# Performance work log

Hardware: AMD Instinct MI355X
Metric: run time of the kernel (lower is better)

The kernel has to match this reference:

```python
import jax, jax.numpy as jnp
import numpy as np

B, S, D, H = 2, 2048, 1024, 16
HD = D // H  # 64


def setup_inputs() -> dict:
    key = jax.random.key(0)
    ks = jax.random.split(key, 10)
    sc = 1.0 / np.sqrt(D)
    return {
        "decoder_hs": jax.random.normal(ks[0], (B, S, D), jnp.float32),
        "encoder_hs": jax.random.normal(ks[1], (B, S, D), jnp.float32),
        "Wq": jax.random.normal(ks[2], (D, D), jnp.float32) * sc,
        "bq": jax.random.normal(ks[3], (D,), jnp.float32) * 0.02,
        "Wk": jax.random.normal(ks[4], (D, D), jnp.float32) * sc,
        "bk": jax.random.normal(ks[5], (D,), jnp.float32) * 0.02,
        "Wv": jax.random.normal(ks[6], (D, D), jnp.float32) * sc,
        "bv": jax.random.normal(ks[7], (D,), jnp.float32) * 0.02,
        "Wp": jax.random.normal(ks[8], (D, D), jnp.float32) * sc,
        "bp": jax.random.normal(ks[9], (D,), jnp.float32) * 0.02,
    }


def reference(decoder_hs, encoder_hs, Wq, bq, Wk, bk, Wv, bv, Wp, bp):
    b, s, d = decoder_hs.shape
    # torch nn.Linear: y = x @ W.T + b, W is [out, in]
    q = decoder_hs @ Wq.T + bq
    k = encoder_hs @ Wk.T + bk
    v = encoder_hs @ Wv.T + bv
    # head split: [b, s, d] -> [b, h, s, hd]
    q = q.reshape(b, s, H, HD).transpose(0, 2, 1, 3)
    k = k.reshape(b, s, H, HD).transpose(0, 2, 1, 3)
    v = v.reshape(b, s, H, HD).transpose(0, 2, 1, 3)
    scale = 1.0 / np.sqrt(HD).astype(np.float32)
    att = jnp.einsum('bhqd,bhkd->bhqk', q, k) * scale
    att = jax.nn.softmax(att, axis=-1)
    y = jnp.einsum('bhqk,bhkd->bhqd', att, v)
    y = y.transpose(0, 2, 1, 3).reshape(b, s, d)
    return y @ Wp.T + bp
```

## Files before the change

kernel.cpp:

```cpp
#include <hip/hip_runtime.h>
#include <hip/hip_bf16.h>
#include <cstdint>
#include <cstddef>

#define BB 2
#define SS 2048
#define DD 1024
#define HH 16
#define HD 64

typedef __attribute__((ext_vector_type(8))) short bf16x8;
typedef __attribute__((ext_vector_type(4))) short bf16x4;
typedef __attribute__((ext_vector_type(4))) float f32x4;

#define MFMA16(va, vb, c) __builtin_amdgcn_mfma_f32_16x16x16bf16_1k(va, vb, c, 0, 0, 0)

#define GLL(g, l) __builtin_amdgcn_global_load_lds( \
    (const __attribute__((address_space(1))) void*)(g), \
    (__attribute__((address_space(3))) void*)(l), 16, 0, 0)

__device__ __forceinline__ short f2bf_fast(float f) {
    uint32_t u = __float_as_uint(f);
    u += 0x7FFF + ((u >> 16) & 1);
    return (short)(u >> 16);
}
__device__ __forceinline__ uint32_t pack_bf2(float a, float b) {
    uint32_t ua = __float_as_uint(a), ub = __float_as_uint(b);
    ua += 0x7FFF + ((ua >> 16) & 1);
    ub += 0x7FFF + ((ub >> 16) & 1);
    return (ua >> 16) | (ub & 0xFFFF0000u);
}
__device__ __forceinline__ bf16x8 cvt8(const float* __restrict__ p) {
    float4 a = *(const float4*)p;
    float4 b = *(const float4*)(p + 4);
    union { uint32_t d[4]; bf16x8 v; } r;
    r.d[0] = pack_bf2(a.x, a.y);
    r.d[1] = pack_bf2(a.z, a.w);
    r.d[2] = pack_bf2(b.x, b.y);
    r.d[3] = pack_bf2(b.z, b.w);
    return r.v;
}

__global__ __launch_bounds__(256) void cvt6_kernel(
    const float* __restrict__ s0, const float* __restrict__ s1,
    const float* __restrict__ s2, const float* __restrict__ s3,
    const float* __restrict__ s4, const float* __restrict__ s5,
    short* __restrict__ d0, short* __restrict__ d1, short* __restrict__ d2,
    short* __restrict__ d3, short* __restrict__ d4, short* __restrict__ d5)
{
    const int z = blockIdx.z;
    const float* s = (z == 0) ? s0 : (z == 1) ? s1 : (z == 2) ? s2
                   : (z == 3) ? s3 : (z == 4) ? s4 : s5;
    short* d = (z == 0) ? d0 : (z == 1) ? d1 : (z == 2) ? d2
             : (z == 3) ? d3 : (z == 4) ? d4 : d5;
    const int n8 = (z < 2) ? (BB * SS * DD / 8) : (DD * DD / 8);
    const int id = blockIdx.x * 256 + threadIdx.x;
    if (id >= n8) return;
    bf16x8 r = cvt8(s + (size_t)id * 8);
    *(uint4*)(d + (size_t)id * 8) = *(uint4*)&r;
}

template<int BF>
__global__ __launch_bounds__(256, 3) void qkv_gemm_kernel(
    const void* __restrict__ dec, const void* __restrict__ enc,
    const void* __restrict__ Wq, const void* __restrict__ Wk,
    const void* __restrict__ Wv,
    const float* __restrict__ bq, const float* __restrict__ bk,
    const float* __restrict__ bv,
    short* __restrict__ Qo, short* __restrict__ Ko, short* __restrict__ Vo)
{
    __shared__ short As[128 * 32];
    __shared__ short Bs[128 * 32];

    const int z = blockIdx.z;
    const void* Xv = (z == 0) ? dec : enc;
    const void* Wp_ = (z == 0) ? Wq : (z == 1) ? Wk : Wv;
    const float* bias = (z == 0) ? bq : (z == 1) ? bk : bv;
    short* Yo = (z == 0) ? Qo : (z == 1) ? Ko : Vo;

    const int t = threadIdx.x;
    const int lane = t & 63, wv = t >> 6;
    const int lr = lane & 15, quad = lane >> 4;
    const int wm = wv >> 1, wn = wv & 1;
    const int m0 = blockIdx.y * 128;
    const int n0 = blockIdx.x * 128;
    const int K = DD;

    f32x4 acc[4][4];
    #pragma unroll
    for (int i = 0; i < 4; i++)
        #pragma unroll
        for (int j = 0; j < 4; j++) acc[i][j] = (f32x4){0.f, 0.f, 0.f, 0.f};

    for (int kb = 0; kb < K; kb += 32) {
        __syncthreads();
        if (BF) {
            const short* Xb = (const short*)Xv;
            const short* Wb = (const short*)Wp_;
            #pragma unroll
            for (int c = 0; c < 2; c++) {
                int r0 = wv * 32 + c * 16;
                int r = r0 + (lane >> 2), ch = (lane & 3) * 8;
                GLL(Xb + (size_t)(m0 + r) * K + kb + ch, &As[r0 * 32]);
                GLL(Wb + (size_t)(n0 + r) * K + kb + ch, &Bs[r0 * 32]);
            }
        } else {
            const float* Xf = (const float*)Xv;
            const float* Wf = (const float*)Wp_;
            #pragma unroll
            for (int c = 0; c < 2; c++) {
                int id = t + c * 256;
                int r = id >> 2, c8 = (id & 3) * 8;
                *(bf16x8*)&As[r * 32 + c8] = cvt8(Xf + (size_t)(m0 + r) * K + kb + c8);
                *(bf16x8*)&Bs[r * 32 + c8] = cvt8(Wf + (size_t)(n0 + r) * K + kb + c8);
            }
        }
        __syncthreads();

        bf16x8 af[4], bfr[4];
        #pragma unroll
        for (int mi = 0; mi < 4; mi++)
            af[mi] = *(const bf16x8*)&As[(wm * 64 + mi * 16 + lr) * 32 + quad * 8];
        #pragma unroll
        for (int ni = 0; ni < 4; ni++)
            bfr[ni] = *(const bf16x8*)&Bs[(wn * 64 + ni * 16 + lr) * 32 + quad * 8];
        #pragma unroll
        for (int mi = 0; mi < 4; mi++)
            #pragma unroll
            for (int ni = 0; ni < 4; ni++)
                acc[mi][ni] = __builtin_amdgcn_mfma_f32_16x16x32_bf16(
                    af[mi], bfr[ni], acc[mi][ni], 0, 0, 0);
    }

    if (z < 2) {
        #pragma unroll
        for (int ni = 0; ni < 4; ni++) {
            int col = n0 + wn * 64 + ni * 16 + lr;
            int h = col >> 6, hd = col & 63;
            float bvv = bias[col];
            #pragma unroll
            for (int mi = 0; mi < 4; mi++) {
                #pragma unroll
                for (int r2 = 0; r2 < 4; r2++) {
                    int row = m0 + wm * 64 + mi * 16 + quad * 4 + r2;
                    int b = row >> 11, s = row & 2047;
                    float v = acc[mi][ni][r2] + bvv;
                    size_t off = ((size_t)(b * HH + h) * SS + s) * HD + hd;
                    Yo[off] = f2bf_fast(v);
                }
            }
        }
    } else {
        #pragma unroll
        for (int ni = 0; ni < 4; ni++) {
            int col = n0 + wn * 64 + ni * 16 + lr;
            int h = col >> 6, hd = col & 63;
            float bvv = bias[col];
            #pragma unroll
            for (int mi = 0; mi < 4; mi++) {
                int s0 = m0 + wm * 64 + mi * 16 + quad * 4;
                int b = s0 >> 11, s = s0 & 2047;
                union { uint32_t d[2]; } u;
                u.d[0] = pack_bf2(acc[mi][ni][0] + bvv, acc[mi][ni][1] + bvv);
                u.d[1] = pack_bf2(acc[mi][ni][2] + bvv, acc[mi][ni][3] + bvv);
                size_t off = ((size_t)(b * HH + h) * HD + hd) * SS + s;
                *(uint2*)(Yo + off) = *(uint2*)&u;
            }
        }
    }
}

template<int WBF>
__global__ __launch_bounds__(256, 2) void proj_gemm_kernel(
    const short* __restrict__ X,
    const void* __restrict__ W, const float* __restrict__ bias,
    float* __restrict__ Y)
{
    __shared__ short As[64 * 32];
    __shared__ short Bs[128 * 32];

    const int t = threadIdx.x;
    const int lane = t & 63, wv = t >> 6;
    const int lr = lane & 15, quad = lane >> 4;
    const int wm = wv >> 1, wn = wv & 1;
    const int m0 = blockIdx.y * 64;
    const int n0 = blockIdx.x * 128;
    const int K = DD, N = DD;

    f32x4 acc[2][4];
    #pragma unroll
    for (int i = 0; i < 2; i++)
        #pragma unroll
        for (int j = 0; j < 4; j++) acc[i][j] = (f32x4){0.f, 0.f, 0.f, 0.f};

    for (int kb = 0; kb < K; kb += 32) {
        __syncthreads();
        {
            int r0 = wv * 16;
            int r = r0 + (lane >> 2), ch = (lane & 3) * 8;
            GLL(X + (size_t)(m0 + r) * K + kb + ch, &As[r0 * 32]);
        }
        if (WBF) {
            const short* Wb = (const short*)W;
            #pragma unroll
            for (int c = 0; c < 2; c++) {
                int r0 = wv * 32 + c * 16;
                int r = r0 + (lane >> 2), ch = (lane & 3) * 8;
                GLL(Wb + (size_t)(n0 + r) * K + kb + ch, &Bs[r0 * 32]);
            }
        } else {
            const float* Wf = (const float*)W;
            #pragma unroll
            for (int c = 0; c < 2; c++) {
                int id = t + c * 256;
                int r = id >> 2, c8 = (id & 3) * 8;
                *(bf16x8*)&Bs[r * 32 + c8] = cvt8(Wf + (size_t)(n0 + r) * K + kb + c8);
            }
        }
        __syncthreads();

        bf16x8 af[2], bfr[4];
        #pragma unroll
        for (int mi = 0; mi < 2; mi++)
            af[mi] = *(const bf16x8*)&As[(wm * 32 + mi * 16 + lr) * 32 + quad * 8];
        #pragma unroll
        for (int ni = 0; ni < 4; ni++)
            bfr[ni] = *(const bf16x8*)&Bs[(wn * 64 + ni * 16 + lr) * 32 + quad * 8];
        #pragma unroll
        for (int mi = 0; mi < 2; mi++)
            #pragma unroll
            for (int ni = 0; ni < 4; ni++)
                acc[mi][ni] = __builtin_amdgcn_mfma_f32_16x16x32_bf16(
                    af[mi], bfr[ni], acc[mi][ni], 0, 0, 0);
    }

    #pragma unroll
    for (int ni = 0; ni < 4; ni++) {
        int col = n0 + wn * 64 + ni * 16 + lr;
        float bvv = bias[col];
        #pragma unroll
        for (int mi = 0; mi < 2; mi++) {
            #pragma unroll
            for (int r2 = 0; r2 < 4; r2++) {
                int row = m0 + wm * 32 + mi * 16 + quad * 4 + r2;
                Y[(size_t)row * N + col] = acc[mi][ni][r2] + bvv;
            }
        }
    }
}

__global__ __launch_bounds__(256, 2) void attn_kernel(
    const short* __restrict__ Q,
    const short* __restrict__ Kgl,
    const short* __restrict__ Vt_g,
    short* __restrict__ Y)
{
    __shared__ short Ks[128][72];
    __shared__ short Vt[64][136];

    const int t = threadIdx.x;
    const int lane = t & 63, w = t >> 6;
    const int lr = lane & 15, quad = lane >> 4;

    const int qt = blockIdx.x & 15;
    const int bh = blockIdx.x >> 4;
    const int b = bh >> 4, h = bh & 15;

    const float C = 0.125f * 1.44269504088896f;

    const short* QpA = Q + ((size_t)bh * SS + qt * 128 + w * 32 + lr) * HD;
    const short* QpB = QpA + 16 * HD;
    bf16x8 qfA0 = *(const bf16x8*)(QpA + quad * 8);
    bf16x8 qfA1 = *(const bf16x8*)(QpA + 32 + quad * 8);
    bf16x8 qfB0 = *(const bf16x8*)(QpB + quad * 8);
    bf16x8 qfB1 = *(const bf16x8*)(QpB + 32 + quad * 8);

    f32x4 oA[4], oB[4];
    #pragma unroll
    for (int i = 0; i < 4; i++) {
        oA[i] = (f32x4){0.f, 0.f, 0.f, 0.f};
        oB[i] = (f32x4){0.f, 0.f, 0.f, 0.f};
    }
    float lsumA = 0.f, lsumB = 0.f;

    const uint4* Kg0 = (const uint4*)(Kgl + (size_t)bh * SS * HD);
    const short* Vg0 = Vt_g + (size_t)bh * HD * SS;

    for (int kt = 0; kt < SS / 128; kt++) {
        __syncthreads();
        const uint4* Kg = Kg0 + (size_t)kt * 128 * 8;
        #pragma unroll
        for (int c = 0; c < 4; c++) {
            int id = t + c * 256;
            int row = id >> 3, h8 = id & 7;
            *(uint4*)&Ks[row][h8 * 8] = Kg[id];
        }
        #pragma unroll
        for (int c = 0; c < 4; c++) {
            int id = t + c * 256;
            int hd = id >> 4, s16 = id & 15;
            *(uint4*)&Vt[hd][s16 * 8] =
                *(const uint4*)(Vg0 + (size_t)hd * SS + kt * 128 + s16 * 8);
        }
        __syncthreads();

        f32x4 scA[8], scB[8];
        #pragma unroll
        for (int nt = 0; nt < 8; nt++) {
            bf16x8 kf0 = *(const bf16x8*)&Ks[nt * 16 + lr][quad * 8];
            bf16x8 kf1 = *(const bf16x8*)&Ks[nt * 16 + lr][32 + quad * 8];
            scA[nt] = __builtin_amdgcn_mfma_f32_16x16x32_bf16(
                kf0, qfA0, (f32x4){0.f, 0.f, 0.f, 0.f}, 0, 0, 0);
            scA[nt] = __builtin_amdgcn_mfma_f32_16x16x32_bf16(kf1, qfA1, scA[nt], 0, 0, 0);
            scB[nt] = __builtin_amdgcn_mfma_f32_16x16x32_bf16(
                kf0, qfB0, (f32x4){0.f, 0.f, 0.f, 0.f}, 0, 0, 0);
            scB[nt] = __builtin_amdgcn_mfma_f32_16x16x32_bf16(kf1, qfB1, scB[nt], 0, 0, 0);
        }

        bf16x4 pbA[8], pbB[8];
        #pragma unroll
        for (int nt = 0; nt < 8; nt++) {
            float a0 = __builtin_amdgcn_exp2f(scA[nt][0] * C);
            float a1 = __builtin_amdgcn_exp2f(scA[nt][1] * C);
            float a2 = __builtin_amdgcn_exp2f(scA[nt][2] * C);
            float a3 = __builtin_amdgcn_exp2f(scA[nt][3] * C);
            lsumA += (a0 + a1) + (a2 + a3);
            union { uint32_t d[2]; bf16x4 v; } ua;
            ua.d[0] = pack_bf2(a0, a1);
            ua.d[1] = pack_bf2(a2, a3);
            pbA[nt] = ua.v;
            float b0 = __builtin_amdgcn_exp2f(scB[nt][0] * C);
            float b1 = __builtin_amdgcn_exp2f(scB[nt][1] * C);
            float b2 = __builtin_amdgcn_exp2f(scB[nt][2] * C);
            float b3 = __builtin_amdgcn_exp2f(scB[nt][3] * C);
            lsumB += (b0 + b1) + (b2 + b3);
            union { uint32_t d[2]; bf16x4 v; } ub;
            ub.d[0] = pack_bf2(b0, b1);
            ub.d[1] = pack_bf2(b2, b3);
            pbB[nt] = ub.v;
        }

        #pragma unroll
        for (int dt = 0; dt < 4; dt++) {
            #pragma unroll
            for (int nt = 0; nt < 8; nt++) {
                bf16x4 va = *(const bf16x4*)&Vt[dt * 16 + lr][nt * 16 + quad * 4];
                oA[dt] = MFMA16(va, pbA[nt], oA[dt]);
                oB[dt] = MFMA16(va, pbB[nt], oB[dt]);
            }
        }
    }

    lsumA += __shfl_xor(lsumA, 16, 64);
    lsumA += __shfl_xor(lsumA, 32, 64);
    lsumB += __shfl_xor(lsumB, 16, 64);
    lsumB += __shfl_xor(lsumB, 32, 64);
    float invA = 1.0f / lsumA, invB = 1.0f / lsumB;

    const int srowA = qt * 128 + w * 32 + lr;
    short* YpA = Y + ((size_t)b * SS + srowA) * DD + h * 64 + quad * 4;
    short* YpB = YpA + 16 * DD;
    #pragma unroll
    for (int dt = 0; dt < 4; dt++) {
        union { uint32_t d[2]; } ua;
        ua.d[0] = pack_bf2(oA[dt][0] * invA, oA[dt][1] * invA);
        ua.d[1] = pack_bf2(oA[dt][2] * invA, oA[dt][3] * invA);
        *(uint2*)(YpA + dt * 16) = *(uint2*)&ua;
        union { uint32_t d[2]; } ub;
        ub.d[0] = pack_bf2(oB[dt][0] * invB, oB[dt][1] * invB);
        ub.d[1] = pack_bf2(oB[dt][2] * invB, oB[dt][3] * invB);
        *(uint2*)(YpB + dt * 16) = *(uint2*)&ub;
    }
}

extern "C" void kernel_launch(void* const* d_in, const int* in_sizes, int n_in,
                              void* d_out, int out_size, void* d_ws, size_t ws_size,
                              hipStream_t stream) {
    const float* dec = (const float*)d_in[0];
    const float* enc = (const float*)d_in[1];
    const float* Wq  = (const float*)d_in[2];
    const float* bq  = (const float*)d_in[3];
    const float* Wk  = (const float*)d_in[4];
    const float* bk  = (const float*)d_in[5];
    const float* Wv  = (const float*)d_in[6];
    const float* bv  = (const float*)d_in[7];
    const float* Wp  = (const float*)d_in[8];
    const float* bp  = (const float*)d_in[9];

    const size_t per = (size_t)BB * HH * SS * HD;
    const size_t wsz = (size_t)DD * DD;
    short* ws = (short*)d_ws;
    short* Qb  = ws;
    short* Kb  = ws + per;
    short* Vtb = ws + 2 * per;
    short* Yb  = ws + 3 * per;

    dim3 qkv_grid(DD / 128, (BB * SS) / 128, 3);
    dim3 proj_grid(DD / 128, (BB * SS) / 64);
    const int attn_blocks = BB * HH * (SS / 128);

    const size_t need = (6 * per + 4 * wsz) * sizeof(short);
    if (ws_size >= need) {
        short* decb = ws + 4 * per;
        short* encb = ws + 5 * per;
        short* Wqb  = ws + 6 * per;
        short* Wkb  = Wqb + wsz;
        short* Wvb  = Wqb + 2 * wsz;
        short* Wpb  = Wqb + 3 * wsz;
        cvt6_kernel<<<dim3((BB * SS * DD / 8 + 255) / 256, 1, 6), 256, 0, stream>>>(
            dec, enc, Wq, Wk, Wv, Wp, decb, encb, Wqb, Wkb, Wvb, Wpb);
        qkv_gemm_kernel<1><<<qkv_grid, 256, 0, stream>>>(
            decb, encb, Wqb, Wkb, Wvb, bq, bk, bv, Qb, Kb, Vtb);
        attn_kernel<<<attn_blocks, 256, 0, stream>>>(Qb, Kb, Vtb, Yb);
        proj_gemm_kernel<1><<<proj_grid, 256, 0, stream>>>(Yb, Wpb, bp, (float*)d_out);
    } else {
        qkv_gemm_kernel<0><<<qkv_grid, 256, 0, stream>>>(
            dec, enc, Wq, Wk, Wv, bq, bk, bv, Qb, Kb, Vtb);
        attn_kernel<<<attn_blocks, 256, 0, stream>>>(Qb, Kb, Vtb, Yb);
        proj_gemm_kernel<0><<<proj_grid, 256, 0, stream>>>(Yb, Wp, bp, (float*)d_out);
    }
}
```

Measured before the change: 215.8 us.

## Double-buffer K/V tiles with async global-to-LDS loads and XOR swizzle

After: 212.3 us. About the same (-1.6%).

```diff
diff --git a/kernel.cpp b/kernel.cpp
--- a/kernel.cpp
+++ b/kernel.cpp
@@ -255,15 +255,18 @@
     const short* __restrict__ Vt_g,
     short* __restrict__ Y)
 {
-    __shared__ short Ks[128][72];
-    __shared__ short Vt[64][136];
+    __shared__ short Ks[2][128][64];
+    __shared__ short Vt[2][64][128];
 
     const int t = threadIdx.x;
     const int lane = t & 63, w = t >> 6;
     const int lr = lane & 15, quad = lane >> 4;
-
-    const int qt = blockIdx.x & 15;
-    const int bh = blockIdx.x >> 4;
+    const int e = lr & 7;
+
+    const int bid = blockIdx.x;
+    const int slot = bid >> 3;
+    const int bh = ((slot >> 4) << 3) + (bid & 7);
+    const int qt = slot & 15;
     const int b = bh >> 4, h = bh & 15;
 
     const float C = 0.125f * 1.44269504088896f;
@@ -283,32 +286,39 @@
     }
     float lsumA = 0.f, lsumB = 0.f;
 
-    const uint4* Kg0 = (const uint4*)(Kgl + (size_t)bh * SS * HD);
-    const short* Vg0 = Vt_g + (size_t)bh * HD * SS;
-
+    const short* Kb = Kgl + (size_t)bh * SS * HD;
+    const short* Vb = Vt_g + (size_t)bh * HD * SS;
+
+    auto stage = [&](int kt1, int nb) {
+        #pragma unroll
+        for (int c = 0; c < 4; c++) {
+            int r0 = w * 32 + c * 8;
+            int r  = r0 + (lane >> 3);
+            int sc = ((lane & 7) ^ (r & 7)) * 8;
+            GLL(Kb + (size_t)(kt1 * 128 + r) * 64 + sc, &Ks[nb][r0][0]);
+        }
+        #pragma unroll
+        for (int c = 0; c < 4; c++) {
+            int h0 = w * 16 + c * 4;
+            int hd = h0 + (lane >> 4);
+            int s16 = (lane & 15) ^ (hd & 7);
+            GLL(Vb + (size_t)hd * SS + kt1 * 128 + s16 * 8, &Vt[nb][h0][0]);
+        }
+    };
+
+    stage(0, 0);
+    __syncthreads();
+
+    int cur = 0;
     for (int kt = 0; kt < SS / 128; kt++) {
-        __syncthreads();
-        const uint4* Kg = Kg0 + (size_t)kt * 128 * 8;
-        #pragma unroll
-        for (int c = 0; c < 4; c++) {
-            int id = t + c * 256;
-            int row = id >> 3, h8 = id & 7;
-            *(uint4*)&Ks[row][h8 * 8] = Kg[id];
-        }
-        #pragma unroll
-        for (int c = 0; c < 4; c++) {
-            int id = t + c * 256;
-            int hd = id >> 4, s16 = id & 15;
-            *(uint4*)&Vt[hd][s16 * 8] =
-                *(const uint4*)(Vg0 + (size_t)hd * SS + kt * 128 + s16 * 8);
-        }
-        __syncthreads();
+        if (kt + 1 < SS / 128) stage(kt + 1, cur ^ 1);
 
         f32x4 scA[8], scB[8];
         #pragma unroll
         for (int nt = 0; nt < 8; nt++) {
-            bf16x8 kf0 = *(const bf16x8*)&Ks[nt * 16 + lr][quad * 8];
-            bf16x8 kf1 = *(const bf16x8*)&Ks[nt * 16 + lr][32 + quad * 8];
+            const short* krow = &Ks[cur][nt * 16 + lr][0];
+            bf16x8 kf0 = *(const bf16x8*)&krow[(quad ^ e) * 8];
+            bf16x8 kf1 = *(const bf16x8*)&krow[((quad + 4) ^ e) * 8];
             scA[nt] = __builtin_amdgcn_mfma_f32_16x16x32_bf16(
                 kf0, qfA0, (f32x4){0.f, 0.f, 0.f, 0.f}, 0, 0, 0);
             scA[nt] = __builtin_amdgcn_mfma_f32_16x16x32_bf16(kf1, qfA1, scA[nt], 0, 0, 0);
@@ -342,13 +352,18 @@
 
         #pragma unroll
         for (int dt = 0; dt < 4; dt++) {
+            const short* vrow = &Vt[cur][dt * 16 + lr][0];
             #pragma unroll
             for (int nt = 0; nt < 8; nt++) {
-                bf16x4 va = *(const bf16x4*)&Vt[dt * 16 + lr][nt * 16 + quad * 4];
+                int ch = (nt * 2 + (quad >> 1)) ^ e;
+                bf16x4 va = *(const bf16x4*)&vrow[ch * 8 + (quad & 1) * 4];
                 oA[dt] = MFMA16(va, pbA[nt], oA[dt]);
                 oB[dt] = MFMA16(va, pbB[nt], oB[dt]);
             }
         }
+
+        __syncthreads();
+        cur ^= 1;
     }
 
     lsumA += __shfl_xor(lsumA, 16, 64);
```
